# Kernel optimization log

Measured on AMD Instinct MI355X. Metric: run time of the kernel, lower is better.

## Reference

```python
import jax, jax.numpy as jnp
import numpy as np

N = 50000      # num nodes
E = 800000     # num edges (avg degree 16)
F_IN = 64      # num_node_features
D = 64         # layer_hidden_dim (= out_channels per layer)
H = 8          # num_heads
C = D // H     # head_dim = 8
L = 5          # num_gnn_layers


def setup_inputs() -> dict:
    key = jax.random.key(0)
    ks = jax.random.split(key, 8)
    x = jax.random.normal(ks[0], (N, F_IN), jnp.float32)
    edge_index = jax.random.randint(ks[1], (2, E), 0, N, dtype=jnp.int32)
    # input embedding Linear(F_IN, D): weight stored as [in, out]
    W_in = jax.random.normal(ks[2], (F_IN, D), jnp.float32) * 0.1
    b_in = jnp.zeros((D,), jnp.float32)
    # per-layer GAT params, stacked over L layers
    lin_w = jax.random.normal(ks[3], (L, D, D), jnp.float32) * 0.1
    lin_b = jnp.zeros((L, D), jnp.float32)
    att = jax.random.normal(ks[4], (L, H, 2 * C), jnp.float32) * 0.1
    out_bias = jnp.zeros((L, D), jnp.float32)
    ln_g = jnp.ones((L, D), jnp.float32)
    ln_b = jnp.zeros((L, D), jnp.float32)
    return {"x": x, "edge_index": edge_index, "W_in": W_in, "b_in": b_in,
            "lin_w": lin_w, "lin_b": lin_b, "att": att, "out_bias": out_bias,
            "ln_g": ln_g, "ln_b": ln_b}


def _gat_layer(h, src, dst, Wl, bl, al, ob, g, b):
    # h: [N, D] -> per-head features [N, H, C]
    hp = (h @ Wl + bl).reshape(N, H, C)
    xi = hp[dst]          # [E, H, C] target-node features (x_i)
    xj = hp[src]          # [E, H, C] source-node features (x_j)
    # cat([x_i, x_j]) . att  == x_i . att[:, :C] + x_j . att[:, C:]
    alpha = jnp.einsum('ehc,hc->eh', xi, al[:, :C]) + \
            jnp.einsum('ehc,hc->eh', xj, al[:, C:])          # [E, H]
    alpha = jax.nn.leaky_relu(alpha, negative_slope=0.2)
    # segment softmax over target index (numerically stable)
    m = jax.ops.segment_max(alpha, dst, num_segments=N)      # [N, H]
    ea = jnp.exp(alpha - m[dst])
    s = jax.ops.segment_sum(ea, dst, num_segments=N)         # [N, H]
    w = ea / (s[dst] + 1e-16)                                # [E, H]
    # message = x_j * alpha, aggr='add'
    agg = jax.ops.segment_sum(xj * w[:, :, None], dst, num_segments=N)  # [N, H, C]
    out = agg.reshape(N, H * C) + ob
    out = jax.nn.elu(out)
    # LayerNorm over feature dim (eval mode: dropout = identity)
    mu = out.mean(-1, keepdims=True)
    var = out.var(-1, keepdims=True)
    return (out - mu) * jax.lax.rsqrt(var + 1e-5) * g + b


def reference(x, edge_index, W_in, b_in, lin_w, lin_b, att, out_bias, ln_g, ln_b):
    src = edge_index[0]
    dst = edge_index[1]   # PyG source_to_target: index = edge_index[1]
    h = jax.nn.relu(x @ W_in + b_in)
    for l in range(L):
        h = _gat_layer(h, src, dst, lin_w[l], lin_b[l], att[l],
                       out_bias[l], ln_g[l], ln_b[l])
    return h
```

## Files before the change

kernel.cpp:

```cpp
#include <hip/hip_runtime.h>
#include <hip/hip_bf16.h>

#define DD 64
#define LL 5
#define KPAD 64
#define L2E 1.4426950408889634f

typedef __attribute__((ext_vector_type(8))) short short8;
typedef __attribute__((ext_vector_type(4))) float float4v;

__device__ __forceinline__ short f2bf_bits(float f) {
    __hip_bfloat16 h = __float2bfloat16(f);
    return *reinterpret_cast<short*>(&h);
}
__device__ __forceinline__ float bfbits2f(short s) {
    __hip_bfloat16 h = *reinterpret_cast<__hip_bfloat16*>(&s);
    return __bfloat162float(h);
}

__device__ __forceinline__ int xcd_swz(int b, int nb) {
    int q = nb >> 3, r = nb & 7;
    int x = b & 7, i = b >> 3;
    return (x < r ? x * (q + 1) : r * (q + 1) + (x - r) * q) + i;
}

__device__ __forceinline__ int sniffw(const unsigned short* xb) {
    int lane = threadIdx.x & 63;
    int e = (xb[lane * 2] >> 7) & 0xFF;
    return __any(e >= 134) ? 1 : 0;
}

__global__ void allcvt_k(const void* __restrict__ x, const void* __restrict__ W_in,
                         const void* __restrict__ b_in, const void* __restrict__ lw,
                         const void* __restrict__ lb, const void* __restrict__ att,
                         const void* __restrict__ ob, const void* __restrict__ lg,
                         const void* __restrict__ lbb,
                         unsigned short* __restrict__ xhi, unsigned short* __restrict__ xlo,
                         float* __restrict__ wts,
                         unsigned short* __restrict__ whiT, unsigned short* __restrict__ wloT,
                         int* __restrict__ deg,
                         int nelem, int nxb, int n) {
    int bid = blockIdx.x;
    int fl = sniffw((const unsigned short*)x);
    if (bid < nxb) {
        int i = bid * 256 + threadIdx.x;
        if (i < nelem) {
            float v = fl ? ((const float*)x)[i] : (float)((const __hip_bfloat16*)x)[i];
            short hi = f2bf_bits(v);
            xhi[i] = (unsigned short)hi;
            xlo[i] = (unsigned short)f2bf_bits(v - bfbits2f(hi));
        }
    } else if (bid < nxb + 104) {
        int i = (bid - nxb) * 256 + threadIdx.x;
        if (i >= 26560) return;
        const void* p; int o;
        if      (i < 4096)  { p = W_in; o = i; }
        else if (i < 4160)  { p = b_in; o = i - 4096; }
        else if (i < 24640) { p = lw;   o = i - 4160; }
        else if (i < 24960) { p = lb;   o = i - 24640; }
        else if (i < 25600) { p = att;  o = i - 24960; }
        else if (i < 25920) { p = ob;   o = i - 25600; }
        else if (i < 26240) { p = lg;   o = i - 25920; }
        else                { p = lbb;  o = i - 26240; }
        wts[i] = fl ? ((const float*)p)[o] : (float)((const __hip_bfloat16*)p)[o];
    } else if (bid < nxb + 104 + 96) {
        int i = (bid - nxb - 104) * 256 + threadIdx.x;
        if (i >= 6 * 4096) return;
        const void* p; int o;
        if (i < 4096) { p = W_in; o = i; } else { p = lw; o = i - 4096; }
        float v = fl ? ((const float*)p)[o] : (float)((const __hip_bfloat16*)p)[o];
        short hi = f2bf_bits(v);
        short lo = f2bf_bits(v - bfbits2f(hi));
        int mat = i >> 12, rem = i & 4095, k = rem >> 6, col = rem & 63;
        int t = mat * 4096 + col * 64 + k;
        whiT[t] = (unsigned short)hi;
        wloT[t] = (unsigned short)lo;
    } else {
        int i = (bid - nxb - 104 - 96) * 256 + threadIdx.x;
        if (i < n) deg[i] = 0;
    }
}

__global__ void csrpad_k(const int* __restrict__ src, const int* __restrict__ dst,
                         int* __restrict__ deg, unsigned short* __restrict__ csr_pad,
                         int e, int psize, int n) {
    int p = blockIdx.x & 7;
    int chunk = blockIdx.x >> 3;
    int lo = p * psize;
    int hi = min(lo + psize, n);
    int base = chunk * 2048 + threadIdx.x;
#pragma unroll
    for (int k = 0; k < 8; ++k) {
        int i = base + k * 256;
        if (i < e) {
            int d = dst[i];
            if (d >= lo && d < hi) {
                int slot = atomicAdd(&deg[d], 1);
                if (slot < KPAD) csr_pad[d * KPAD + slot] = (unsigned short)src[i];
            }
        }
    }
}

__device__ __forceinline__ void gemm_from_lds(
        const unsigned short (*AH)[72], const unsigned short (*AL)[72],
        const unsigned short* __restrict__ Whi, const unsigned short* __restrict__ Wlo,
        const float* __restrict__ bias, const float* __restrict__ Att,
        unsigned short* __restrict__ hp_out, float* __restrict__ bd,
        float* __restrict__ ss, int base, int n) {
    int lane = threadIdx.x & 63;
    int wave = threadIdx.x >> 6;
    int m = lane & 15;
    int q = lane >> 4;
    int coln = wave * 16 + m;

    short8 ah0 = *reinterpret_cast<const short8*>(&AH[m][q * 8]);
    short8 ah1 = *reinterpret_cast<const short8*>(&AH[m][32 + q * 8]);
    short8 al0 = *reinterpret_cast<const short8*>(&AL[m][q * 8]);
    short8 al1 = *reinterpret_cast<const short8*>(&AL[m][32 + q * 8]);

    short8 bh0 = *reinterpret_cast<const short8*>(Whi + coln * 64 + q * 8);
    short8 bh1 = *reinterpret_cast<const short8*>(Whi + coln * 64 + 32 + q * 8);
    short8 bl0 = *reinterpret_cast<const short8*>(Wlo + coln * 64 + q * 8);
    short8 bl1 = *reinterpret_cast<const short8*>(Wlo + coln * 64 + 32 + q * 8);

    float4v acc = {0.f, 0.f, 0.f, 0.f};
    acc = __builtin_amdgcn_mfma_f32_16x16x32_bf16(ah0, bh0, acc, 0, 0, 0);
    acc = __builtin_amdgcn_mfma_f32_16x16x32_bf16(al0, bh0, acc, 0, 0, 0);
    acc = __builtin_amdgcn_mfma_f32_16x16x32_bf16(ah0, bl0, acc, 0, 0, 0);
    acc = __builtin_amdgcn_mfma_f32_16x16x32_bf16(ah1, bh1, acc, 0, 0, 0);
    acc = __builtin_amdgcn_mfma_f32_16x16x32_bf16(al1, bh1, acc, 0, 0, 0);
    acc = __builtin_amdgcn_mfma_f32_16x16x32_bf16(ah1, bl1, acc, 0, 0, 0);

    float bc = bias[coln];
    int c_ = m & 7;
    int hh = 2 * wave + (m >> 3);
    float attd = Att[hh * 16 + c_];
    float atts = Att[hh * 16 + 8 + c_];
#pragma unroll
    for (int r = 0; r < 4; ++r) {
        int rr = base + q * 4 + r;
        float v = acc[r] + bc;
        short vb = f2bf_bits(v);
        float vr = bfbits2f(vb);
        if (rr < n) hp_out[(size_t)rr * 64 + coln] = (unsigned short)vb;
        float bdv = vr * attd;
        float ssv = vr * atts;
        bdv += __shfl_xor(bdv, 1, 64);
        bdv += __shfl_xor(bdv, 2, 64);
        bdv += __shfl_xor(bdv, 4, 64);
        ssv += __shfl_xor(ssv, 1, 64);
        ssv += __shfl_xor(ssv, 2, 64);
        ssv += __shfl_xor(ssv, 4, 64);
        if ((m & 7) == 0 && rr < n) {
            bd[rr * 8 + hh] = bdv * L2E;
            ss[rr * 8 + hh] = ssv * L2E;
        }
    }
}

__global__ void __launch_bounds__(256) k0_k(const unsigned short* __restrict__ xhi,
                                            const unsigned short* __restrict__ xlo,
                                            const unsigned short* __restrict__ whiT,
                                            const unsigned short* __restrict__ wloT,
                                            const float* __restrict__ bias_in,
                                            const float* __restrict__ bias_l0,
                                            const float* __restrict__ att0,
                                            unsigned short* __restrict__ hp_out,
                                            float* __restrict__ bd, float* __restrict__ ss,
                                            int n) {
    __shared__ unsigned short AH[16][72];
    __shared__ unsigned short AL[16][72];
    int lane = threadIdx.x & 63;
    int wave = threadIdx.x >> 6;
    int m = lane & 15;
    int q = lane >> 4;
    int coln = wave * 16 + m;
    int base = xcd_swz(blockIdx.x, gridDim.x) * 16;

    {
        int arow = min(base + m, n - 1);
        const unsigned short* ap = xhi + (size_t)arow * 64 + q * 8;
        const unsigned short* alp = xlo + (size_t)arow * 64 + q * 8;
        short8 ah0 = *reinterpret_cast<const short8*>(ap);
        short8 ah1 = *reinterpret_cast<const short8*>(ap + 32);
        short8 al0 = *reinterpret_cast<const short8*>(alp);
        short8 al1 = *reinterpret_cast<const short8*>(alp + 32);
        short8 bh0 = *reinterpret_cast<const short8*>(whiT + coln * 64 + q * 8);
        short8 bh1 = *reinterpret_cast<const short8*>(whiT + coln * 64 + 32 + q * 8);
        short8 bl0 = *reinterpret_cast<const short8*>(wloT + coln * 64 + q * 8);
        short8 bl1 = *reinterpret_cast<const short8*>(wloT + coln * 64 + 32 + q * 8);
        float4v acc = {0.f, 0.f, 0.f, 0.f};
        acc = __builtin_amdgcn_mfma_f32_16x16x32_bf16(ah0, bh0, acc, 0, 0, 0);
        acc = __builtin_amdgcn_mfma_f32_16x16x32_bf16(al0, bh0, acc, 0, 0, 0);
        acc = __builtin_amdgcn_mfma_f32_16x16x32_bf16(ah0, bl0, acc, 0, 0, 0);
        acc = __builtin_amdgcn_mfma_f32_16x16x32_bf16(ah1, bh1, acc, 0, 0, 0);
        acc = __builtin_amdgcn_mfma_f32_16x16x32_bf16(al1, bh1, acc, 0, 0, 0);
        acc = __builtin_amdgcn_mfma_f32_16x16x32_bf16(ah1, bl1, acc, 0, 0, 0);
        float bc = bias_in[coln];
#pragma unroll
        for (int r = 0; r < 4; ++r) {
            float v = fmaxf(acc[r] + bc, 0.f);
            short hi = f2bf_bits(v);
            AH[q * 4 + r][coln] = (unsigned short)hi;
            AL[q * 4 + r][coln] = (unsigned short)f2bf_bits(v - bfbits2f(hi));
        }
    }
    __syncthreads();
    gemm_from_lds(AH, AL, whiT + 4096, wloT + 4096, bias_l0, att0,
                  hp_out, bd, ss, base, n);
}

#define EXJ(W, j) { unsigned ws_ = (e1 & 4) ? ((e1 & 2) ? W.w : W.z) : ((e1 & 2) ? W.y : W.x); \
    j = (e1 & 1) ? (int)(ws_ >> 16) : (int)(ws_ & 0xffffu); j = min(j, nm1); }
#define EXG(W, g0, g1) { unsigned d0_ = (qt & 2) ? W.y : W.x; unsigned d1_ = (qt & 2) ? W.w : W.z; \
    g0 = (qt & 1) ? (int)(d0_ >> 16) : (int)(d0_ & 0xffffu); \
    g1 = (qt & 1) ? (int)(d1_ >> 16) : (int)(d1_ & 0xffffu); \
    g0 = min(g0, nm1); g1 = min(g1, nm1); }
#define FMA4(V, W, A0, A1, A2, A3) \
    A0 = fmaf(__int_as_float((int)(V.x << 16)), W, A0); \
    A1 = fmaf(__int_as_float((int)(V.x & 0xffff0000u)), W, A1); \
    A2 = fmaf(__int_as_float((int)(V.y << 16)), W, A2); \
    A3 = fmaf(__int_as_float((int)(V.y & 0xffff0000u)), W, A3);

#define ISSUE(c, WA, WB) \
    int jA_##c; EXJ(WA, jA_##c) \
    int jB_##c; EXJ(WB, jB_##c) \
    float ssA_##c = ss_in[jA_##c * 8 + h1]; \
    float ssB_##c = ss_in[jB_##c * 8 + h1]; \
    int gA0_##c; int gA1_##c; EXG(WA, gA0_##c, gA1_##c) \
    int gB0_##c; int gB1_##c; EXG(WB, gB0_##c, gB1_##c) \
    uint2 vA0_##c = *reinterpret_cast<const uint2*>(hpbf + (size_t)gA0_##c * 64 + fq4); \
    uint2 vA1_##c = *reinterpret_cast<const uint2*>(hpbf + (size_t)gA1_##c * 64 + fq4); \
    uint2 vB0_##c = *reinterpret_cast<const uint2*>(hpbf + (size_t)gB0_##c * 64 + fq4); \
    uint2 vB1_##c = *reinterpret_cast<const uint2*>(hpbf + (size_t)gB1_##c * 64 + fq4);

#define COMP(c) { \
    int slot_ = c * 8 + e1; \
    if (c < ncA) { \
        float aa_ = bhA + ssA_##c; aa_ = (aa_ > 0.f) ? aa_ : 0.2f * aa_; \
        float wg_ = (slot_ < ddA) ? exp2f(fminf(aa_, 60.f)) : 0.f; \
        sA += wg_; \
        float w0_ = __int_as_float(__builtin_amdgcn_ds_bpermute(bb, __float_as_int(wg_))); \
        float w1_ = __int_as_float(__builtin_amdgcn_ds_bpermute(bb + 128, __float_as_int(wg_))); \
        FMA4(vA0_##c, w0_, aA0, aA1, aA2, aA3) \
        FMA4(vA1_##c, w1_, aA0, aA1, aA2, aA3) \
    } \
    if (c < ncB) { \
        float aa_ = bhB + ssB_##c; aa_ = (aa_ > 0.f) ? aa_ : 0.2f * aa_; \
        float wg_ = (slot_ < ddB) ? exp2f(fminf(aa_, 60.f)) : 0.f; \
        sB += wg_; \
        float w0_ = __int_as_float(__builtin_amdgcn_ds_bpermute(bb, __float_as_int(wg_))); \
        float w1_ = __int_as_float(__builtin_amdgcn_ds_bpermute(bb + 128, __float_as_int(wg_))); \
        FMA4(vB0_##c, w0_, aB0, aB1, aB2, aB3) \
        FMA4(vB1_##c, w1_, aB0, aB1, aB2, aB3) \
    } }

__device__ __forceinline__ void gat_half(
        const unsigned short* __restrict__ hpbf,
        const float* __restrict__ ss_in,
        const unsigned short* __restrict__ csr,
        int uA, int uB, int ddA, int ddB, float bhA, float bhB,
        int e1, int h1, int qt, int fq4, int bb, int nm1,
        int qselA, int qselB,
        float& r0, float& r1, float& r2, float& r3, float& rsum) {
    const uint4* cA = reinterpret_cast<const uint4*>(csr + (size_t)uA * KPAD);
    const uint4* cB = reinterpret_cast<const uint4*>(csr + (size_t)uB * KPAD);
    uint4 wa0 = cA[0], wa1 = cA[1], wa2 = cA[2], wa3 = cA[3];
    uint4 wb0 = cB[0], wb1 = cB[1], wb2 = cB[2], wb3 = cB[3];
    int ncA = (ddA + 7) >> 3;
    int ncB = (ddB + 7) >> 3;
    int ncm = max(ncA, ncB);

    float sA = 0.f, sB = 0.f;
    float aA0 = 0.f, aA1 = 0.f, aA2 = 0.f, aA3 = 0.f;
    float aB0 = 0.f, aB1 = 0.f, aB2 = 0.f, aB3 = 0.f;

    if (ncm <= 2) {
        ISSUE(0, wa0, wb0)
        ISSUE(1, wa1, wb1)
        COMP(0)
        COMP(1)
    } else if (ncm == 3) {
        ISSUE(0, wa0, wb0)
        ISSUE(1, wa1, wb1)
        COMP(0)
        ISSUE(2, wa2, wb2)
        COMP(1)
        COMP(2)
    } else {
        ISSUE(0, wa0, wb0)
        ISSUE(1, wa1, wb1)
        COMP(0)
        ISSUE(2, wa2, wb2)
        COMP(1)
        ISSUE(3, wa3, wb3)
        COMP(2)
        COMP(3)
        for (int c = 4; c < ncm; ++c) {
            uint4 wac = cA[c];
            uint4 wbc = cB[c];
            int jA; EXJ(wac, jA)
            int jB; EXJ(wbc, jB)
            float ssAv = ss_in[jA * 8 + h1];
            float ssBv = ss_in[jB * 8 + h1];
            int gA0; int gA1; EXG(wac, gA0, gA1)
            int gB0; int gB1; EXG(wbc, gB0, gB1)
            uint2 vA0 = *reinterpret_cast<const uint2*>(hpbf + (size_t)gA0 * 64 + fq4);
            uint2 vA1 = *reinterpret_cast<const uint2*>(hpbf + (size_t)gA1 * 64 + fq4);
            uint2 vB0 = *reinterpret_cast<const uint2*>(hpbf + (size_t)gB0 * 64 + fq4);
            uint2 vB1 = *reinterpret_cast<const uint2*>(hpbf + (size_t)gB1 * 64 + fq4);
            int slot_ = c * 8 + e1;
            if (c < ncA) {
                float aa_ = bhA + ssAv; aa_ = (aa_ > 0.f) ? aa_ : 0.2f * aa_;
                float wg_ = (slot_ < ddA) ? exp2f(fminf(aa_, 60.f)) : 0.f;
                sA += wg_;
                float w0_ = __int_as_float(__builtin_amdgcn_ds_bpermute(bb, __float_as_int(wg_)));
                float w1_ = __int_as_float(__builtin_amdgcn_ds_bpermute(bb + 128, __float_as_int(wg_)));
                FMA4(vA0, w0_, aA0, aA1, aA2, aA3)
                FMA4(vA1, w1_, aA0, aA1, aA2, aA3)
            }
            if (c < ncB) {
                float aa_ = bhB + ssBv; aa_ = (aa_ > 0.f) ? aa_ : 0.2f * aa_;
                float wg_ = (slot_ < ddB) ? exp2f(fminf(aa_, 60.f)) : 0.f;
                sB += wg_;
                float w0_ = __int_as_float(__builtin_amdgcn_ds_bpermute(bb, __float_as_int(wg_)));
                float w1_ = __int_as_float(__builtin_amdgcn_ds_bpermute(bb + 128, __float_as_int(wg_)));
                FMA4(vB0, w0_, aB0, aB1, aB2, aB3)
                FMA4(vB1, w1_, aB0, aB1, aB2, aB3)
            }
        }
    }

    float ssumA = sA;
    ssumA += __shfl_xor(ssumA, 8, 64);
    ssumA += __shfl_xor(ssumA, 16, 64);
    ssumA += __shfl_xor(ssumA, 32, 64);
    float ssumB = sB;
    ssumB += __shfl_xor(ssumB, 8, 64);
    ssumB += __shfl_xor(ssumB, 16, 64);
    ssumB += __shfl_xor(ssumB, 32, 64);

    aA0 += __shfl_xor(aA0, 16, 64); aA0 += __shfl_xor(aA0, 32, 64);
    aA1 += __shfl_xor(aA1, 16, 64); aA1 += __shfl_xor(aA1, 32, 64);
    aA2 += __shfl_xor(aA2, 16, 64); aA2 += __shfl_xor(aA2, 32, 64);
    aA3 += __shfl_xor(aA3, 16, 64); aA3 += __shfl_xor(aA3, 32, 64);
    aB0 += __shfl_xor(aB0, 16, 64); aB0 += __shfl_xor(aB0, 32, 64);
    aB1 += __shfl_xor(aB1, 16, 64); aB1 += __shfl_xor(aB1, 32, 64);
    aB2 += __shfl_xor(aB2, 16, 64); aB2 += __shfl_xor(aB2, 32, 64);
    aB3 += __shfl_xor(aB3, 16, 64); aB3 += __shfl_xor(aB3, 32, 64);

    if (qt == qselA) { r0 = aA0; r1 = aA1; r2 = aA2; r3 = aA3; rsum = ssumA; }
    if (qt == qselB) { r0 = aB0; r1 = aB1; r2 = aB2; r3 = aB3; rsum = ssumB; }
}

__global__ void __launch_bounds__(256) layer_k(const unsigned short* __restrict__ hpbf,
                                               const int* __restrict__ deg,
                                               const unsigned short* __restrict__ csr,
                                               const float* __restrict__ bd_in,
                                               const float* __restrict__ ss_in,
                                               const float* __restrict__ ob,
                                               const float* __restrict__ g,
                                               const float* __restrict__ b,
                                               const unsigned short* __restrict__ Wnhi,
                                               const unsigned short* __restrict__ Wnlo,
                                               const float* __restrict__ bias_n,
                                               const float* __restrict__ att_n,
                                               unsigned short* __restrict__ hp_out,
                                               float* __restrict__ bd_out,
                                               float* __restrict__ ss_out,
                                               void* __restrict__ outp,
                                               const unsigned short* __restrict__ xb,
                                               int n, int last) {
    __shared__ unsigned short AH[16][72];
    __shared__ unsigned short AL[16][72];
    int lane = threadIdx.x & 63;
    int wave = threadIdx.x >> 6;
    int base = xcd_swz(blockIdx.x, gridDim.x) * 16;

    int h1 = lane & 7;
    int e1 = lane >> 3;
    int qt = lane >> 4;
    int fq = lane & 15;
    int fq4 = fq * 4;
    int h2 = fq >> 1;
    int bb = qt * 32 + h2 * 4;
    int nm1 = n - 1;

    int fl = last ? sniffw(xb) : 0;

    int nd0 = base + wave * 4;
    int4 dv = *reinterpret_cast<const int4*>(deg + nd0);
    int dd0 = __builtin_amdgcn_readfirstlane((nd0 + 0 < n) ? min(dv.x, KPAD) : 0);
    int dd1 = __builtin_amdgcn_readfirstlane((nd0 + 1 < n) ? min(dv.y, KPAD) : 0);
    int dd2 = __builtin_amdgcn_readfirstlane((nd0 + 2 < n) ? min(dv.z, KPAD) : 0);
    int dd3 = __builtin_amdgcn_readfirstlane((nd0 + 3 < n) ? min(dv.w, KPAD) : 0);
    float bhv0 = bd_in[min(nd0 + 0, nm1) * 8 + h1];
    float bhv1 = bd_in[min(nd0 + 1, nm1) * 8 + h1];
    float bhv2 = bd_in[min(nd0 + 2, nm1) * 8 + h1];
    float bhv3 = bd_in[min(nd0 + 3, nm1) * 8 + h1];
    int u0 = __builtin_amdgcn_readfirstlane(min(nd0 + 0, nm1));
    int u1 = __builtin_amdgcn_readfirstlane(min(nd0 + 1, nm1));
    int u2 = __builtin_amdgcn_readfirstlane(min(nd0 + 2, nm1));
    int u3 = __builtin_amdgcn_readfirstlane(min(nd0 + 3, nm1));

    float r0 = 0.f, r1 = 0.f, r2 = 0.f, r3 = 0.f, rsum = 0.f;

    gat_half(hpbf, ss_in, csr, u0, u1, dd0, dd1, bhv0, bhv1,
             e1, h1, qt, fq4, bb, nm1, 0, 1, r0, r1, r2, r3, rsum);
    gat_half(hpbf, ss_in, csr, u2, u3, dd2, dd3, bhv2, bhv3,
             e1, h1, qt, fq4, bb, nm1, 2, 3, r0, r1, r2, r3, rsum);

    float sh = __int_as_float(
        __builtin_amdgcn_ds_bpermute((qt * 16 + h2) * 4, __float_as_int(rsum)));
    float rinv = __builtin_amdgcn_rcpf(sh + 1e-16f);
    float4 ob4 = ((const float4*)ob)[fq];
    float o0 = r0 * rinv + ob4.x;
    float o1 = r1 * rinv + ob4.y;
    float o2 = r2 * rinv + ob4.z;
    float o3 = r3 * rinv + ob4.w;
    o0 = (o0 > 0.f) ? o0 : exp2f(o0 * L2E) - 1.f;
    o1 = (o1 > 0.f) ? o1 : exp2f(o1 * L2E) - 1.f;
    o2 = (o2 > 0.f) ? o2 : exp2f(o2 * L2E) - 1.f;
    o3 = (o3 > 0.f) ? o3 : exp2f(o3 * L2E) - 1.f;

    float ps = o0 + o1 + o2 + o3;
#pragma unroll
    for (int d = 1; d < 16; d <<= 1) ps += __shfl_xor(ps, d, 64);
    float mu = ps * (1.f / 64.f);
    float d0 = o0 - mu, d1 = o1 - mu, d2v = o2 - mu, d3 = o3 - mu;
    float sq = d0 * d0 + d1 * d1 + d2v * d2v + d3 * d3;
#pragma unroll
    for (int d = 1; d < 16; d <<= 1) sq += __shfl_xor(sq, d, 64);
    float rstd = __builtin_amdgcn_rsqf(sq * (1.f / 64.f) + 1e-5f);
    float4 g4 = ((const float4*)g)[fq];
    float4 b4 = ((const float4*)b)[fq];
    float y0 = d0 * rstd * g4.x + b4.x;
    float y1 = d1 * rstd * g4.y + b4.y;
    float y2 = d2v * rstd * g4.z + b4.z;
    float y3 = d3 * rstd * g4.w + b4.w;

    int onode = nd0 + qt;
    if (!last) {
        int ridx = wave * 4 + qt;
        short hb0 = f2bf_bits(y0), hb1 = f2bf_bits(y1);
        short hb2 = f2bf_bits(y2), hb3 = f2bf_bits(y3);
        unsigned hA = (unsigned short)hb0 | ((unsigned)(unsigned short)hb1 << 16);
        unsigned hB = (unsigned short)hb2 | ((unsigned)(unsigned short)hb3 << 16);
        uint2 yh = {hA, hB};
        unsigned lA = (unsigned short)f2bf_bits(y0 - bfbits2f(hb0)) |
                      ((unsigned)(unsigned short)f2bf_bits(y1 - bfbits2f(hb1)) << 16);
        unsigned lB = (unsigned short)f2bf_bits(y2 - bfbits2f(hb2)) |
                      ((unsigned)(unsigned short)f2bf_bits(y3 - bfbits2f(hb3)) << 16);
        uint2 yl = {lA, lB};
        *reinterpret_cast<uint2*>(&AH[ridx][fq * 4]) = yh;
        *reinterpret_cast<uint2*>(&AL[ridx][fq * 4]) = yl;
    } else if (onode < n) {
        if (fl) {
            float4 y = {y0, y1, y2, y3};
            ((float4*)outp)[(size_t)onode * 16 + fq] = y;
        } else {
            unsigned lo = (unsigned short)f2bf_bits(y0) |
                          ((unsigned)(unsigned short)f2bf_bits(y1) << 16);
            unsigned hi = (unsigned short)f2bf_bits(y2) |
                          ((unsigned)(unsigned short)f2bf_bits(y3) << 16);
            uint2 y = {lo, hi};
            ((uint2*)outp)[(size_t)onode * 16 + fq] = y;
        }
    }

    if (last) return;
    __syncthreads();
    gemm_from_lds(AH, AL, Wnhi, Wnlo, bias_n, att_n, hp_out, bd_out, ss_out, base, n);
}

static void* g_pool = nullptr;
static size_t g_pool_sz = 0;

extern "C" void kernel_launch(void* const* d_in, const int* in_sizes, int n_in,
                              void* d_out, int out_size, void* d_ws, size_t ws_size,
                              hipStream_t stream) {
    const void* x    = d_in[0];
    const int* ei    = (const int*)d_in[1];
    const void* W_in = d_in[2];
    const void* b_in = d_in[3];
    const void* lw   = d_in[4];
    const void* lb   = d_in[5];
    const void* att  = d_in[6];
    const void* ob   = d_in[7];
    const void* lg   = d_in[8];
    const void* lbb  = d_in[9];

    const int n = in_sizes[0] / DD;
    const int e = in_sizes[1] / 2;
    const int* src = ei;
    const int* dst = ei + e;

    auto align256 = [](size_t v) { return (v + 255) & ~(size_t)255; };
    size_t need = 0;
    size_t off_xhi  = need; need += align256((size_t)n * DD * 2);
    size_t off_xlo  = need; need += align256((size_t)n * DD * 2);
    size_t off_hpA  = need; need += align256((size_t)(n + 32) * DD * 2);
    size_t off_hpB  = need; need += align256((size_t)(n + 32) * DD * 2);
    size_t off_deg  = need; need += align256((size_t)(n + 32) * 4);
    size_t off_csr  = need; need += align256((size_t)n * KPAD * 2);
    size_t off_wts  = need; need += align256((size_t)26560 * 4);
    size_t off_bdA  = need; need += align256((size_t)n * 8 * 4);
    size_t off_ssA  = need; need += align256((size_t)n * 8 * 4);
    size_t off_bdB  = need; need += align256((size_t)n * 8 * 4);
    size_t off_ssB  = need; need += align256((size_t)n * 8 * 4);
    size_t off_whi  = need; need += align256((size_t)6 * 4096 * 2);
    size_t off_wlo  = need; need += align256((size_t)6 * 4096 * 2);

    char* ws;
    if (ws_size >= need) {
        ws = (char*)d_ws;
    } else {
        if (g_pool == nullptr || g_pool_sz < need) {
            hipMalloc(&g_pool, need);
            g_pool_sz = need;
        }
        ws = (char*)g_pool;
    }

    unsigned short* xhi = (unsigned short*)(ws + off_xhi);
    unsigned short* xlo = (unsigned short*)(ws + off_xlo);
    unsigned short* hpA = (unsigned short*)(ws + off_hpA);
    unsigned short* hpB = (unsigned short*)(ws + off_hpB);
    int* deg     = (int*)(ws + off_deg);
    unsigned short* csr = (unsigned short*)(ws + off_csr);
    float* wts   = (float*)(ws + off_wts);
    float* bdA   = (float*)(ws + off_bdA);
    float* ssA   = (float*)(ws + off_ssA);
    float* bdB   = (float*)(ws + off_bdB);
    float* ssB   = (float*)(ws + off_ssB);
    unsigned short* whiT = (unsigned short*)(ws + off_whi);
    unsigned short* wloT = (unsigned short*)(ws + off_wlo);

    float* wb_in = wts + 4096;
    float* wlb   = wts + 24640;
    float* watt  = wts + 24960;
    float* wob   = wts + 25600;
    float* wlg   = wts + 25920;
    float* wlbb  = wts + 26240;

    int nelem = n * DD;
    int nxb = (nelem + 255) / 256;
    int degb = (n + 255) / 256;
    allcvt_k<<<nxb + 104 + 96 + degb, 256, 0, stream>>>(
        x, W_in, b_in, lw, lb, att, ob, lg, lbb,
        xhi, xlo, wts, whiT, wloT, deg, nelem, nxb, n);

    int psize = (n + 7) / 8;
    int chunks = (e + 2047) / 2048;
    csrpad_k<<<chunks * 8, 256, 0, stream>>>(src, dst, deg, csr, e, psize, n);

    int nb16 = (n + 15) / 16;
    k0_k<<<nb16, 256, 0, stream>>>(xhi, xlo, whiT, wloT, wb_in, wlb, watt,
                                   hpA, bdA, ssA, n);

    for (int l = 0; l < LL; ++l) {
        int last = (l == LL - 1) ? 1 : 0;
        unsigned short* hin = (l & 1) ? hpB : hpA;
        float* bdi = (l & 1) ? bdB : bdA;
        float* ssi = (l & 1) ? ssB : ssA;
        unsigned short* hout = (l & 1) ? hpA : hpB;
        float* bdo = (l & 1) ? bdA : bdB;
        float* sso = (l & 1) ? ssA : ssB;
        layer_k<<<nb16, 256, 0, stream>>>(
            hin, deg, csr, bdi, ssi,
            wob + (size_t)l * DD, wlg + (size_t)l * DD, wlbb + (size_t)l * DD,
            whiT + (size_t)(l + 2) * 4096, wloT + (size_t)(l + 2) * 4096,
            wlb + (size_t)(l + 1) * DD, watt + (size_t)(l + 1) * 128,
            hout, bdo, sso, d_out, (const unsigned short*)x, n, last);
    }
}
```

Before: 292.2 us.

## Remap GAT aggregation lanes to per-head 16-byte gathers, 32 nodes per block

Restructures the layer kernel's lane mapping so each lane owns one head and one edge slot and gathers all 8 channels of that head with a single 16-byte load. This replaces the paired 8-byte gathers and the ds_bpermute weight broadcasts. Each wave now handles 8 nodes instead of 4, so blocks cover 32 nodes, and a new two-tile MFMA projection routine reuses the loaded weights across both 16-row tiles. The XCD block swizzle is removed. In exchange the kernel holds more accumulator registers and does more cross-lane shuffle reductions, which may lower occupancy.

```diff
diff --git a/kernel.cpp b/kernel.cpp
--- a/kernel.cpp
+++ b/kernel.cpp
@@ -16,12 +16,6 @@
 __device__ __forceinline__ float bfbits2f(short s) {
     __hip_bfloat16 h = *reinterpret_cast<__hip_bfloat16*>(&s);
     return __bfloat162float(h);
-}
-
-__device__ __forceinline__ int xcd_swz(int b, int nb) {
-    int q = nb >> 3, r = nb & 7;
-    int x = b & 7, i = b >> 3;
-    return (x < r ? x * (q + 1) : r * (q + 1) + (x - r) * q) + i;
 }
 
 __device__ __forceinline__ int sniffw(const unsigned short* xb) {
@@ -159,6 +153,67 @@
     }
 }
 
+__device__ __forceinline__ void gemm_from_lds32(
+        const unsigned short (*AH)[72], const unsigned short (*AL)[72],
+        const unsigned short* __restrict__ Whi, const unsigned short* __restrict__ Wlo,
+        const float* __restrict__ bias, const float* __restrict__ Att,
+        unsigned short* __restrict__ hp_out, float* __restrict__ bd,
+        float* __restrict__ ss, int base, int n) {
+    int lane = threadIdx.x & 63;
+    int wave = threadIdx.x >> 6;
+    int m = lane & 15;
+    int q = lane >> 4;
+    int coln = wave * 16 + m;
+
+    short8 bh0 = *reinterpret_cast<const short8*>(Whi + coln * 64 + q * 8);
+    short8 bh1 = *reinterpret_cast<const short8*>(Whi + coln * 64 + 32 + q * 8);
+    short8 bl0 = *reinterpret_cast<const short8*>(Wlo + coln * 64 + q * 8);
+    short8 bl1 = *reinterpret_cast<const short8*>(Wlo + coln * 64 + 32 + q * 8);
+
+    float bc = bias[coln];
+    int c_ = m & 7;
+    int hh = 2 * wave + (m >> 3);
+    float attd = Att[hh * 16 + c_];
+    float atts = Att[hh * 16 + 8 + c_];
+
+#pragma unroll
+    for (int mi = 0; mi < 2; ++mi) {
+        short8 ah0 = *reinterpret_cast<const short8*>(&AH[mi * 16 + m][q * 8]);
+        short8 ah1 = *reinterpret_cast<const short8*>(&AH[mi * 16 + m][32 + q * 8]);
+        short8 al0 = *reinterpret_cast<const short8*>(&AL[mi * 16 + m][q * 8]);
+        short8 al1 = *reinterpret_cast<const short8*>(&AL[mi * 16 + m][32 + q * 8]);
+
+        float4v acc = {0.f, 0.f, 0.f, 0.f};
+        acc = __builtin_amdgcn_mfma_f32_16x16x32_bf16(ah0, bh0, acc, 0, 0, 0);
+        acc = __builtin_amdgcn_mfma_f32_16x16x32_bf16(al0, bh0, acc, 0, 0, 0);
+        acc = __builtin_amdgcn_mfma_f32_16x16x32_bf16(ah0, bl0, acc, 0, 0, 0);
+        acc = __builtin_amdgcn_mfma_f32_16x16x32_bf16(ah1, bh1, acc, 0, 0, 0);
+        acc = __builtin_amdgcn_mfma_f32_16x16x32_bf16(al1, bh1, acc, 0, 0, 0);
+        acc = __builtin_amdgcn_mfma_f32_16x16x32_bf16(ah1, bl1, acc, 0, 0, 0);
+
+#pragma unroll
+        for (int r = 0; r < 4; ++r) {
+            int rr = base + mi * 16 + q * 4 + r;
+            float v = acc[r] + bc;
+            short vb = f2bf_bits(v);
+            float vr = bfbits2f(vb);
+            if (rr < n) hp_out[(size_t)rr * 64 + coln] = (unsigned short)vb;
+            float bdv = vr * attd;
+            float ssv = vr * atts;
+            bdv += __shfl_xor(bdv, 1, 64);
+            bdv += __shfl_xor(bdv, 2, 64);
+            bdv += __shfl_xor(bdv, 4, 64);
+            ssv += __shfl_xor(ssv, 1, 64);
+            ssv += __shfl_xor(ssv, 2, 64);
+            ssv += __shfl_xor(ssv, 4, 64);
+            if ((m & 7) == 0 && rr < n) {
+                bd[rr * 8 + hh] = bdv * L2E;
+                ss[rr * 8 + hh] = ssv * L2E;
+            }
+        }
+    }
+}
+
 __global__ void __launch_bounds__(256) k0_k(const unsigned short* __restrict__ xhi,
                                             const unsigned short* __restrict__ xlo,
                                             const unsigned short* __restrict__ whiT,
@@ -176,7 +231,7 @@
     int m = lane & 15;
     int q = lane >> 4;
     int coln = wave * 16 + m;
-    int base = xcd_swz(blockIdx.x, gridDim.x) * 16;
+    int base = blockIdx.x * 16;
 
     {
         int arow = min(base + m, n - 1);
@@ -213,145 +268,124 @@
 
 #define EXJ(W, j) { unsigned ws_ = (e1 & 4) ? ((e1 & 2) ? W.w : W.z) : ((e1 & 2) ? W.y : W.x); \
     j = (e1 & 1) ? (int)(ws_ >> 16) : (int)(ws_ & 0xffffu); j = min(j, nm1); }
-#define EXG(W, g0, g1) { unsigned d0_ = (qt & 2) ? W.y : W.x; unsigned d1_ = (qt & 2) ? W.w : W.z; \
-    g0 = (qt & 1) ? (int)(d0_ >> 16) : (int)(d0_ & 0xffffu); \
-    g1 = (qt & 1) ? (int)(d1_ >> 16) : (int)(d1_ & 0xffffu); \
-    g0 = min(g0, nm1); g1 = min(g1, nm1); }
-#define FMA4(V, W, A0, A1, A2, A3) \
-    A0 = fmaf(__int_as_float((int)(V.x << 16)), W, A0); \
-    A1 = fmaf(__int_as_float((int)(V.x & 0xffff0000u)), W, A1); \
-    A2 = fmaf(__int_as_float((int)(V.y << 16)), W, A2); \
-    A3 = fmaf(__int_as_float((int)(V.y & 0xffff0000u)), W, A3);
-
-#define ISSUE(c, WA, WB) \
+#define BFLO(d) __int_as_float((int)((d) << 16))
+#define BFHI(d) __int_as_float((int)((d) & 0xffff0000u))
+#define FMA8(V, W, P) \
+    P##0 = fmaf(BFLO(V.x), W, P##0); P##1 = fmaf(BFHI(V.x), W, P##1); \
+    P##2 = fmaf(BFLO(V.y), W, P##2); P##3 = fmaf(BFHI(V.y), W, P##3); \
+    P##4 = fmaf(BFLO(V.z), W, P##4); P##5 = fmaf(BFHI(V.z), W, P##5); \
+    P##6 = fmaf(BFLO(V.w), W, P##6); P##7 = fmaf(BFHI(V.w), W, P##7);
+
+#define PISSUE(c, WA, WB) \
     int jA_##c; EXJ(WA, jA_##c) \
     int jB_##c; EXJ(WB, jB_##c) \
     float ssA_##c = ss_in[jA_##c * 8 + h1]; \
     float ssB_##c = ss_in[jB_##c * 8 + h1]; \
-    int gA0_##c; int gA1_##c; EXG(WA, gA0_##c, gA1_##c) \
-    int gB0_##c; int gB1_##c; EXG(WB, gB0_##c, gB1_##c) \
-    uint2 vA0_##c = *reinterpret_cast<const uint2*>(hpbf + (size_t)gA0_##c * 64 + fq4); \
-    uint2 vA1_##c = *reinterpret_cast<const uint2*>(hpbf + (size_t)gA1_##c * 64 + fq4); \
-    uint2 vB0_##c = *reinterpret_cast<const uint2*>(hpbf + (size_t)gB0_##c * 64 + fq4); \
-    uint2 vB1_##c = *reinterpret_cast<const uint2*>(hpbf + (size_t)gB1_##c * 64 + fq4);
-
-#define COMP(c) { \
+    uint4 vA_##c = *reinterpret_cast<const uint4*>(hpbf + (size_t)jA_##c * 64 + h18); \
+    uint4 vB_##c = *reinterpret_cast<const uint4*>(hpbf + (size_t)jB_##c * 64 + h18);
+
+#define PCOMP(c) { \
     int slot_ = c * 8 + e1; \
     if (c < ncA) { \
         float aa_ = bhA + ssA_##c; aa_ = (aa_ > 0.f) ? aa_ : 0.2f * aa_; \
         float wg_ = (slot_ < ddA) ? exp2f(fminf(aa_, 60.f)) : 0.f; \
-        sA += wg_; \
-        float w0_ = __int_as_float(__builtin_amdgcn_ds_bpermute(bb, __float_as_int(wg_))); \
-        float w1_ = __int_as_float(__builtin_amdgcn_ds_bpermute(bb + 128, __float_as_int(wg_))); \
-        FMA4(vA0_##c, w0_, aA0, aA1, aA2, aA3) \
-        FMA4(vA1_##c, w1_, aA0, aA1, aA2, aA3) \
-    } \
+        sA += wg_; FMA8(vA_##c, wg_, A) } \
     if (c < ncB) { \
         float aa_ = bhB + ssB_##c; aa_ = (aa_ > 0.f) ? aa_ : 0.2f * aa_; \
         float wg_ = (slot_ < ddB) ? exp2f(fminf(aa_, 60.f)) : 0.f; \
-        sB += wg_; \
-        float w0_ = __int_as_float(__builtin_amdgcn_ds_bpermute(bb, __float_as_int(wg_))); \
-        float w1_ = __int_as_float(__builtin_amdgcn_ds_bpermute(bb + 128, __float_as_int(wg_))); \
-        FMA4(vB0_##c, w0_, aB0, aB1, aB2, aB3) \
-        FMA4(vB1_##c, w1_, aB0, aB1, aB2, aB3) \
-    } }
-
-__device__ __forceinline__ void gat_half(
+        sB += wg_; FMA8(vB_##c, wg_, B) } }
+
+__device__ __forceinline__ void gat_pair(
         const unsigned short* __restrict__ hpbf,
         const float* __restrict__ ss_in,
         const unsigned short* __restrict__ csr,
-        int uA, int uB, int ddA, int ddB, float bhA, float bhB,
-        int e1, int h1, int qt, int fq4, int bb, int nm1,
-        int qselA, int qselB,
-        float& r0, float& r1, float& r2, float& r3, float& rsum) {
+        const float* __restrict__ bd_in,
+        int uA, int uB, int ddA, int ddB,
+        int e1, int h1, int h18, int nm1, int selA, int selB,
+        float& r0, float& r1, float& r2, float& r3,
+        float& r4, float& r5, float& r6, float& r7, float& rsum) {
     const uint4* cA = reinterpret_cast<const uint4*>(csr + (size_t)uA * KPAD);
     const uint4* cB = reinterpret_cast<const uint4*>(csr + (size_t)uB * KPAD);
     uint4 wa0 = cA[0], wa1 = cA[1], wa2 = cA[2], wa3 = cA[3];
     uint4 wb0 = cB[0], wb1 = cB[1], wb2 = cB[2], wb3 = cB[3];
+    float bhA = bd_in[uA * 8 + h1];
+    float bhB = bd_in[uB * 8 + h1];
     int ncA = (ddA + 7) >> 3;
     int ncB = (ddB + 7) >> 3;
     int ncm = max(ncA, ncB);
 
     float sA = 0.f, sB = 0.f;
-    float aA0 = 0.f, aA1 = 0.f, aA2 = 0.f, aA3 = 0.f;
-    float aB0 = 0.f, aB1 = 0.f, aB2 = 0.f, aB3 = 0.f;
+    float A0 = 0.f, A1 = 0.f, A2 = 0.f, A3 = 0.f, A4 = 0.f, A5 = 0.f, A6 = 0.f, A7 = 0.f;
+    float B0 = 0.f, B1 = 0.f, B2 = 0.f, B3 = 0.f, B4 = 0.f, B5 = 0.f, B6 = 0.f, B7 = 0.f;
 
     if (ncm <= 2) {
-        ISSUE(0, wa0, wb0)
-        ISSUE(1, wa1, wb1)
-        COMP(0)
-        COMP(1)
+        PISSUE(0, wa0, wb0)
+        PISSUE(1, wa1, wb1)
+        PCOMP(0)
+        PCOMP(1)
     } else if (ncm == 3) {
-        ISSUE(0, wa0, wb0)
-        ISSUE(1, wa1, wb1)
-        COMP(0)
-        ISSUE(2, wa2, wb2)
-        COMP(1)
-        COMP(2)
+        PISSUE(0, wa0, wb0)
+        PISSUE(1, wa1, wb1)
+        PCOMP(0)
+        PISSUE(2, wa2, wb2)
+        PCOMP(1)
+        PCOMP(2)
+    } else if (ncm == 4) {
+        PISSUE(0, wa0, wb0)
+        PISSUE(1, wa1, wb1)
+        PCOMP(0)
+        PISSUE(2, wa2, wb2)
+        PCOMP(1)
+        PISSUE(3, wa3, wb3)
+        PCOMP(2)
+        PCOMP(3)
     } else {
-        ISSUE(0, wa0, wb0)
-        ISSUE(1, wa1, wb1)
-        COMP(0)
-        ISSUE(2, wa2, wb2)
-        COMP(1)
-        ISSUE(3, wa3, wb3)
-        COMP(2)
-        COMP(3)
-        for (int c = 4; c < ncm; ++c) {
+        for (int c = 0; c < ncm; ++c) {
             uint4 wac = cA[c];
             uint4 wbc = cB[c];
             int jA; EXJ(wac, jA)
             int jB; EXJ(wbc, jB)
             float ssAv = ss_in[jA * 8 + h1];
             float ssBv = ss_in[jB * 8 + h1];
-            int gA0; int gA1; EXG(wac, gA0, gA1)
-            int gB0; int gB1; EXG(wbc, gB0, gB1)
-            uint2 vA0 = *reinterpret_cast<const uint2*>(hpbf + (size_t)gA0 * 64 + fq4);
-            uint2 vA1 = *reinterpret_cast<const uint2*>(hpbf + (size_t)gA1 * 64 + fq4);
-            uint2 vB0 = *reinterpret_cast<const uint2*>(hpbf + (size_t)gB0 * 64 + fq4);
-            uint2 vB1 = *reinterpret_cast<const uint2*>(hpbf + (size_t)gB1 * 64 + fq4);
+            uint4 vA = *reinterpret_cast<const uint4*>(hpbf + (size_t)jA * 64 + h18);
+            uint4 vB = *reinterpret_cast<const uint4*>(hpbf + (size_t)jB * 64 + h18);
             int slot_ = c * 8 + e1;
             if (c < ncA) {
                 float aa_ = bhA + ssAv; aa_ = (aa_ > 0.f) ? aa_ : 0.2f * aa_;
                 float wg_ = (slot_ < ddA) ? exp2f(fminf(aa_, 60.f)) : 0.f;
-                sA += wg_;
-                float w0_ = __int_as_float(__builtin_amdgcn_ds_bpermute(bb, __float_as_int(wg_)));
-                float w1_ = __int_as_float(__builtin_amdgcn_ds_bpermute(bb + 128, __float_as_int(wg_)));
-                FMA4(vA0, w0_, aA0, aA1, aA2, aA3)
-                FMA4(vA1, w1_, aA0, aA1, aA2, aA3)
+                sA += wg_; FMA8(vA, wg_, A)
             }
             if (c < ncB) {
                 float aa_ = bhB + ssBv; aa_ = (aa_ > 0.f) ? aa_ : 0.2f * aa_;
                 float wg_ = (slot_ < ddB) ? exp2f(fminf(aa_, 60.f)) : 0.f;
-                sB += wg_;
-                float w0_ = __int_as_float(__builtin_amdgcn_ds_bpermute(bb, __float_as_int(wg_)));
-                float w1_ = __int_as_float(__builtin_amdgcn_ds_bpermute(bb + 128, __float_as_int(wg_)));
-                FMA4(vB0, w0_, aB0, aB1, aB2, aB3)
-                FMA4(vB1, w1_, aB0, aB1, aB2, aB3)
+                sB += wg_; FMA8(vB, wg_, B)
             }
         }
     }
 
-    float ssumA = sA;
-    ssumA += __shfl_xor(ssumA, 8, 64);
-    ssumA += __shfl_xor(ssumA, 16, 64);
-    ssumA += __shfl_xor(ssumA, 32, 64);
-    float ssumB = sB;
-    ssumB += __shfl_xor(ssumB, 8, 64);
-    ssumB += __shfl_xor(ssumB, 16, 64);
-    ssumB += __shfl_xor(ssumB, 32, 64);
-
-    aA0 += __shfl_xor(aA0, 16, 64); aA0 += __shfl_xor(aA0, 32, 64);
-    aA1 += __shfl_xor(aA1, 16, 64); aA1 += __shfl_xor(aA1, 32, 64);
-    aA2 += __shfl_xor(aA2, 16, 64); aA2 += __shfl_xor(aA2, 32, 64);
-    aA3 += __shfl_xor(aA3, 16, 64); aA3 += __shfl_xor(aA3, 32, 64);
-    aB0 += __shfl_xor(aB0, 16, 64); aB0 += __shfl_xor(aB0, 32, 64);
-    aB1 += __shfl_xor(aB1, 16, 64); aB1 += __shfl_xor(aB1, 32, 64);
-    aB2 += __shfl_xor(aB2, 16, 64); aB2 += __shfl_xor(aB2, 32, 64);
-    aB3 += __shfl_xor(aB3, 16, 64); aB3 += __shfl_xor(aB3, 32, 64);
-
-    if (qt == qselA) { r0 = aA0; r1 = aA1; r2 = aA2; r3 = aA3; rsum = ssumA; }
-    if (qt == qselB) { r0 = aB0; r1 = aB1; r2 = aB2; r3 = aB3; rsum = ssumB; }
+    sA += __shfl_xor(sA, 8, 64); sA += __shfl_xor(sA, 16, 64); sA += __shfl_xor(sA, 32, 64);
+    sB += __shfl_xor(sB, 8, 64); sB += __shfl_xor(sB, 16, 64); sB += __shfl_xor(sB, 32, 64);
+    A0 += __shfl_xor(A0, 8, 64); A0 += __shfl_xor(A0, 16, 64); A0 += __shfl_xor(A0, 32, 64);
+    A1 += __shfl_xor(A1, 8, 64); A1 += __shfl_xor(A1, 16, 64); A1 += __shfl_xor(A1, 32, 64);
+    A2 += __shfl_xor(A2, 8, 64); A2 += __shfl_xor(A2, 16, 64); A2 += __shfl_xor(A2, 32, 64);
+    A3 += __shfl_xor(A3, 8, 64); A3 += __shfl_xor(A3, 16, 64); A3 += __shfl_xor(A3, 32, 64);
+    A4 += __shfl_xor(A4, 8, 64); A4 += __shfl_xor(A4, 16, 64); A4 += __shfl_xor(A4, 32, 64);
+    A5 += __shfl_xor(A5, 8, 64); A5 += __shfl_xor(A5, 16, 64); A5 += __shfl_xor(A5, 32, 64);
+    A6 += __shfl_xor(A6, 8, 64); A6 += __shfl_xor(A6, 16, 64); A6 += __shfl_xor(A6, 32, 64);
+    A7 += __shfl_xor(A7, 8, 64); A7 += __shfl_xor(A7, 16, 64); A7 += __shfl_xor(A7, 32, 64);
+    B0 += __shfl_xor(B0, 8, 64); B0 += __shfl_xor(B0, 16, 64); B0 += __shfl_xor(B0, 32, 64);
+    B1 += __shfl_xor(B1, 8, 64); B1 += __shfl_xor(B1, 16, 64); B1 += __shfl_xor(B1, 32, 64);
+    B2 += __shfl_xor(B2, 8, 64); B2 += __shfl_xor(B2, 16, 64); B2 += __shfl_xor(B2, 32, 64);
+    B3 += __shfl_xor(B3, 8, 64); B3 += __shfl_xor(B3, 16, 64); B3 += __shfl_xor(B3, 32, 64);
+    B4 += __shfl_xor(B4, 8, 64); B4 += __shfl_xor(B4, 16, 64); B4 += __shfl_xor(B4, 32, 64);
+    B5 += __shfl_xor(B5, 8, 64); B5 += __shfl_xor(B5, 16, 64); B5 += __shfl_xor(B5, 32, 64);
+    B6 += __shfl_xor(B6, 8, 64); B6 += __shfl_xor(B6, 16, 64); B6 += __shfl_xor(B6, 32, 64);
+    B7 += __shfl_xor(B7, 8, 64); B7 += __shfl_xor(B7, 16, 64); B7 += __shfl_xor(B7, 32, 64);
+
+    if (e1 == selA) { r0 = A0; r1 = A1; r2 = A2; r3 = A3;
+                      r4 = A4; r5 = A5; r6 = A6; r7 = A7; rsum = sA; }
+    if (e1 == selB) { r0 = B0; r1 = B1; r2 = B2; r3 = B3;
+                      r4 = B4; r5 = B5; r6 = B6; r7 = B7; rsum = sB; }
 }
 
 __global__ void __launch_bounds__(256) layer_k(const unsigned short* __restrict__ hpbf,
@@ -372,106 +406,132 @@
                                                void* __restrict__ outp,
                                                const unsigned short* __restrict__ xb,
                                                int n, int last) {
-    __shared__ unsigned short AH[16][72];
-    __shared__ unsigned short AL[16][72];
+    __shared__ unsigned short AH[32][72];
+    __shared__ unsigned short AL[32][72];
     int lane = threadIdx.x & 63;
     int wave = threadIdx.x >> 6;
-    int base = xcd_swz(blockIdx.x, gridDim.x) * 16;
+    int base = blockIdx.x * 32;
 
     int h1 = lane & 7;
     int e1 = lane >> 3;
-    int qt = lane >> 4;
-    int fq = lane & 15;
-    int fq4 = fq * 4;
-    int h2 = fq >> 1;
-    int bb = qt * 32 + h2 * 4;
+    int h18 = h1 * 8;
     int nm1 = n - 1;
 
     int fl = last ? sniffw(xb) : 0;
 
-    int nd0 = base + wave * 4;
-    int4 dv = *reinterpret_cast<const int4*>(deg + nd0);
-    int dd0 = __builtin_amdgcn_readfirstlane((nd0 + 0 < n) ? min(dv.x, KPAD) : 0);
-    int dd1 = __builtin_amdgcn_readfirstlane((nd0 + 1 < n) ? min(dv.y, KPAD) : 0);
-    int dd2 = __builtin_amdgcn_readfirstlane((nd0 + 2 < n) ? min(dv.z, KPAD) : 0);
-    int dd3 = __builtin_amdgcn_readfirstlane((nd0 + 3 < n) ? min(dv.w, KPAD) : 0);
-    float bhv0 = bd_in[min(nd0 + 0, nm1) * 8 + h1];
-    float bhv1 = bd_in[min(nd0 + 1, nm1) * 8 + h1];
-    float bhv2 = bd_in[min(nd0 + 2, nm1) * 8 + h1];
-    float bhv3 = bd_in[min(nd0 + 3, nm1) * 8 + h1];
+    int nd0 = base + wave * 8;
+    int4 dva = *reinterpret_cast<const int4*>(deg + nd0);
+    int4 dvb = *reinterpret_cast<const int4*>(deg + nd0 + 4);
+    int dd0 = __builtin_amdgcn_readfirstlane((nd0 + 0 < n) ? min(dva.x, KPAD) : 0);
+    int dd1 = __builtin_amdgcn_readfirstlane((nd0 + 1 < n) ? min(dva.y, KPAD) : 0);
+    int dd2 = __builtin_amdgcn_readfirstlane((nd0 + 2 < n) ? min(dva.z, KPAD) : 0);
+    int dd3 = __builtin_amdgcn_readfirstlane((nd0 + 3 < n) ? min(dva.w, KPAD) : 0);
+    int dd4 = __builtin_amdgcn_readfirstlane((nd0 + 4 < n) ? min(dvb.x, KPAD) : 0);
+    int dd5 = __builtin_amdgcn_readfirstlane((nd0 + 5 < n) ? min(dvb.y, KPAD) : 0);
+    int dd6 = __builtin_amdgcn_readfirstlane((nd0 + 6 < n) ? min(dvb.z, KPAD) : 0);
+    int dd7 = __builtin_amdgcn_readfirstlane((nd0 + 7 < n) ? min(dvb.w, KPAD) : 0);
     int u0 = __builtin_amdgcn_readfirstlane(min(nd0 + 0, nm1));
     int u1 = __builtin_amdgcn_readfirstlane(min(nd0 + 1, nm1));
     int u2 = __builtin_amdgcn_readfirstlane(min(nd0 + 2, nm1));
     int u3 = __builtin_amdgcn_readfirstlane(min(nd0 + 3, nm1));
-
-    float r0 = 0.f, r1 = 0.f, r2 = 0.f, r3 = 0.f, rsum = 0.f;
-
-    gat_half(hpbf, ss_in, csr, u0, u1, dd0, dd1, bhv0, bhv1,
-             e1, h1, qt, fq4, bb, nm1, 0, 1, r0, r1, r2, r3, rsum);
-    gat_half(hpbf, ss_in, csr, u2, u3, dd2, dd3, bhv2, bhv3,
-             e1, h1, qt, fq4, bb, nm1, 2, 3, r0, r1, r2, r3, rsum);
-
-    float sh = __int_as_float(
-        __builtin_amdgcn_ds_bpermute((qt * 16 + h2) * 4, __float_as_int(rsum)));
-    float rinv = __builtin_amdgcn_rcpf(sh + 1e-16f);
-    float4 ob4 = ((const float4*)ob)[fq];
-    float o0 = r0 * rinv + ob4.x;
-    float o1 = r1 * rinv + ob4.y;
-    float o2 = r2 * rinv + ob4.z;
-    float o3 = r3 * rinv + ob4.w;
+    int u4 = __builtin_amdgcn_readfirstlane(min(nd0 + 4, nm1));
+    int u5 = __builtin_amdgcn_readfirstlane(min(nd0 + 5, nm1));
+    int u6 = __builtin_amdgcn_readfirstlane(min(nd0 + 6, nm1));
+    int u7 = __builtin_amdgcn_readfirstlane(min(nd0 + 7, nm1));
+
+    float r0 = 0.f, r1 = 0.f, r2 = 0.f, r3 = 0.f;
+    float r4 = 0.f, r5 = 0.f, r6 = 0.f, r7 = 0.f, rsum = 0.f;
+
+    gat_pair(hpbf, ss_in, csr, bd_in, u0, u1, dd0, dd1, e1, h1, h18, nm1, 0, 1,
+             r0, r1, r2, r3, r4, r5, r6, r7, rsum);
+    gat_pair(hpbf, ss_in, csr, bd_in, u2, u3, dd2, dd3, e1, h1, h18, nm1, 2, 3,
+             r0, r1, r2, r3, r4, r5, r6, r7, rsum);
+    gat_pair(hpbf, ss_in, csr, bd_in, u4, u5, dd4, dd5, e1, h1, h18, nm1, 4, 5,
+             r0, r1, r2, r3, r4, r5, r6, r7, rsum);
+    gat_pair(hpbf, ss_in, csr, bd_in, u6, u7, dd6, dd7, e1, h1, h18, nm1, 6, 7,
+             r0, r1, r2, r3, r4, r5, r6, r7, rsum);
+
+    float rinv = __builtin_amdgcn_rcpf(rsum + 1e-16f);
+    float4 oba = ((const float4*)ob)[h1 * 2];
+    float4 obb = ((const float4*)ob)[h1 * 2 + 1];
+    float o0 = r0 * rinv + oba.x;
+    float o1 = r1 * rinv + oba.y;
+    float o2 = r2 * rinv + oba.z;
+    float o3 = r3 * rinv + oba.w;
+    float o4 = r4 * rinv + obb.x;
+    float o5 = r5 * rinv + obb.y;
+    float o6 = r6 * rinv + obb.z;
+    float o7 = r7 * rinv + obb.w;
     o0 = (o0 > 0.f) ? o0 : exp2f(o0 * L2E) - 1.f;
     o1 = (o1 > 0.f) ? o1 : exp2f(o1 * L2E) - 1.f;
     o2 = (o2 > 0.f) ? o2 : exp2f(o2 * L2E) - 1.f;
     o3 = (o3 > 0.f) ? o3 : exp2f(o3 * L2E) - 1.f;
-
-    float ps = o0 + o1 + o2 + o3;
-#pragma unroll
-    for (int d = 1; d < 16; d <<= 1) ps += __shfl_xor(ps, d, 64);
+    o4 = (o4 > 0.f) ? o4 : exp2f(o4 * L2E) - 1.f;
+    o5 = (o5 > 0.f) ? o5 : exp2f(o5 * L2E) - 1.f;
+    o6 = (o6 > 0.f) ? o6 : exp2f(o6 * L2E) - 1.f;
+    o7 = (o7 > 0.f) ? o7 : exp2f(o7 * L2E) - 1.f;
+
+    float ps = o0 + o1 + o2 + o3 + o4 + o5 + o6 + o7;
+    ps += __shfl_xor(ps, 1, 64); ps += __shfl_xor(ps, 2, 64); ps += __shfl_xor(ps, 4, 64);
     float mu = ps * (1.f / 64.f);
-    float d0 = o0 - mu, d1 = o1 - mu, d2v = o2 - mu, d3 = o3 - mu;
-    float sq = d0 * d0 + d1 * d1 + d2v * d2v + d3 * d3;
-#pragma unroll
-    for (int d = 1; d < 16; d <<= 1) sq += __shfl_xor(sq, d, 64);
+    float d0 = o0 - mu, d1 = o1 - mu, d2 = o2 - mu, d3 = o3 - mu;
+    float d4 = o4 - mu, d5 = o5 - mu, d6 = o6 - mu, d7 = o7 - mu;
+    float sq = d0 * d0 + d1 * d1 + d2 * d2 + d3 * d3 + d4 * d4 + d5 * d5 + d6 * d6 + d7 * d7;
+    sq += __shfl_xor(sq, 1, 64); sq += __shfl_xor(sq, 2, 64); sq += __shfl_xor(sq, 4, 64);
     float rstd = __builtin_amdgcn_rsqf(sq * (1.f / 64.f) + 1e-5f);
-    float4 g4 = ((const float4*)g)[fq];
-    float4 b4 = ((const float4*)b)[fq];
-    float y0 = d0 * rstd * g4.x + b4.x;
-    float y1 = d1 * rstd * g4.y + b4.y;
-    float y2 = d2v * rstd * g4.z + b4.z;
-    float y3 = d3 * rstd * g4.w + b4.w;
-
-    int onode = nd0 + qt;
+    float4 g4a = ((const float4*)g)[h1 * 2];
+    float4 g4b = ((const float4*)g)[h1 * 2 + 1];
+    float4 b4a = ((const float4*)b)[h1 * 2];
+    float4 b4b = ((const float4*)b)[h1 * 2 + 1];
+    float y0 = d0 * rstd * g4a.x + b4a.x;
+    float y1 = d1 * rstd * g4a.y + b4a.y;
+    float y2 = d2 * rstd * g4a.z + b4a.z;
+    float y3 = d3 * rstd * g4a.w + b4a.w;
+    float y4 = d4 * rstd * g4b.x + b4b.x;
+    float y5 = d5 * rstd * g4b.y + b4b.y;
+    float y6 = d6 * rstd * g4b.z + b4b.z;
+    float y7 = d7 * rstd * g4b.w + b4b.w;
+
+    int onode = nd0 + e1;
     if (!last) {
-        int ridx = wave * 4 + qt;
-        short hb0 = f2bf_bits(y0), hb1 = f2bf_bits(y1);
-        short hb2 = f2bf_bits(y2), hb3 = f2bf_bits(y3);
-        unsigned hA = (unsigned short)hb0 | ((unsigned)(unsigned short)hb1 << 16);
-        unsigned hB = (unsigned short)hb2 | ((unsigned)(unsigned short)hb3 << 16);
-        uint2 yh = {hA, hB};
-        unsigned lA = (unsigned short)f2bf_bits(y0 - bfbits2f(hb0)) |
-                      ((unsigned)(unsigned short)f2bf_bits(y1 - bfbits2f(hb1)) << 16);
-        unsigned lB = (unsigned short)f2bf_bits(y2 - bfbits2f(hb2)) |
-                      ((unsigned)(unsigned short)f2bf_bits(y3 - bfbits2f(hb3)) << 16);
-        uint2 yl = {lA, lB};
-        *reinterpret_cast<uint2*>(&AH[ridx][fq * 4]) = yh;
-        *reinterpret_cast<uint2*>(&AL[ridx][fq * 4]) = yl;
+        int ridx = wave * 8 + e1;
+        short t0 = f2bf_bits(y0), t1 = f2bf_bits(y1), t2 = f2bf_bits(y2), t3 = f2bf_bits(y3);
+        short t4 = f2bf_bits(y4), t5 = f2bf_bits(y5), t6 = f2bf_bits(y6), t7 = f2bf_bits(y7);
+        uint4 yh;
+        yh.x = (unsigned short)t0 | ((unsigned)(unsigned short)t1 << 16);
+        yh.y = (unsigned short)t2 | ((unsigned)(unsigned short)t3 << 16);
+        yh.z = (unsigned short)t4 | ((unsigned)(unsigned short)t5 << 16);
+        yh.w = (unsigned short)t6 | ((unsigned)(unsigned short)t7 << 16);
+        uint4 yl;
+        yl.x = (unsigned short)f2bf_bits(y0 - bfbits2f(t0)) |
+               ((unsigned)(unsigned short)f2bf_bits(y1 - bfbits2f(t1)) << 16);
+        yl.y = (unsigned short)f2bf_bits(y2 - bfbits2f(t2)) |
+               ((unsigned)(unsigned short)f2bf_bits(y3 - bfbits2f(t3)) << 16);
+        yl.z = (unsigned short)f2bf_bits(y4 - bfbits2f(t4)) |
+               ((unsigned)(unsigned short)f2bf_bits(y5 - bfbits2f(t5)) << 16);
+        yl.w = (unsigned short)f2bf_bits(y6 - bfbits2f(t6)) |
+               ((unsigned)(unsigned short)f2bf_bits(y7 - bfbits2f(t7)) << 16);
+        *reinterpret_cast<uint4*>(&AH[ridx][h18]) = yh;
+        *reinterpret_cast<uint4*>(&AL[ridx][h18]) = yl;
     } else if (onode < n) {
         if (fl) {
-            float4 y = {y0, y1, y2, y3};
-            ((float4*)outp)[(size_t)onode * 16 + fq] = y;
+            float4 ya = {y0, y1, y2, y3};
+            float4 yb = {y4, y5, y6, y7};
+            ((float4*)outp)[(size_t)onode * 16 + h1 * 2] = ya;
+            ((float4*)outp)[(size_t)onode * 16 + h1 * 2 + 1] = yb;
         } else {
-            unsigned lo = (unsigned short)f2bf_bits(y0) |
-                          ((unsigned)(unsigned short)f2bf_bits(y1) << 16);
-            unsigned hi = (unsigned short)f2bf_bits(y2) |
-                          ((unsigned)(unsigned short)f2bf_bits(y3) << 16);
-            uint2 y = {lo, hi};
-            ((uint2*)outp)[(size_t)onode * 16 + fq] = y;
+            uint4 yo;
+            yo.x = (unsigned short)f2bf_bits(y0) | ((unsigned)(unsigned short)f2bf_bits(y1) << 16);
+            yo.y = (unsigned short)f2bf_bits(y2) | ((unsigned)(unsigned short)f2bf_bits(y3) << 16);
+            yo.z = (unsigned short)f2bf_bits(y4) | ((unsigned)(unsigned short)f2bf_bits(y5) << 16);
+            yo.w = (unsigned short)f2bf_bits(y6) | ((unsigned)(unsigned short)f2bf_bits(y7) << 16);
+            ((uint4*)outp)[(size_t)onode * 8 + h1] = yo;
         }
     }
 
     if (last) return;
     __syncthreads();
-    gemm_from_lds(AH, AL, Wnhi, Wnlo, bias_n, att_n, hp_out, bd_out, ss_out, base, n);
+    gemm_from_lds32(AH, AL, Wnhi, Wnlo, bias_n, att_n, hp_out, bd_out, ss_out, base, n);
 }
 
 static void* g_pool = nullptr;
@@ -559,6 +619,7 @@
     k0_k<<<nb16, 256, 0, stream>>>(xhi, xlo, whiT, wloT, wb_in, wlb, watt,
                                    hpA, bdA, ssA, n);
 
+    int nb32 = (n + 31) / 32;
     for (int l = 0; l < LL; ++l) {
         int last = (l == LL - 1) ? 1 : 0;
         unsigned short* hin = (l & 1) ? hpB : hpA;
@@ -567,7 +628,7 @@
         unsigned short* hout = (l & 1) ? hpA : hpB;
         float* bdo = (l & 1) ? bdA : bdB;
         float* sso = (l & 1) ? ssA : ssB;
-        layer_k<<<nb16, 256, 0, stream>>>(
+        layer_k<<<nb32, 256, 0, stream>>>(
             hin, deg, csr, bdi, ssi,
             wob + (size_t)l * DD, wlg + (size_t)l * DD, wlbb + (size_t)l * DD,
             whiT + (size_t)(l + 2) * 4096, wloT + (size_t)(l + 2) * 4096,
```

New measurement: 303.4 us. 1.04x slower.
